# Optimization experiments

Measured on AMD Instinct MI355X. Metric: run time of the kernel, lower is better.

## Reference

```python
import jax, jax.numpy as jnp
import numpy as np
from jax import lax

CHUNK = 256  # points of the query set processed per step; intermediate is [B, CHUNK, M]


def _nn_min(x, y):
    """For each point in x [B,N,3], squared distance + index of nearest point in y [B,M,3].
    Chunked over N so the full [B,N,M] distance matrix is never materialized."""
    B, N, _ = x.shape
    y2 = jnp.sum(y * y, axis=-1)  # [B, M]
    K = N // CHUNK
    xr = jnp.swapaxes(x.reshape(B, K, CHUNK, 3), 0, 1)  # [K, B, CHUNK, 3]

    def chunk_fn(xc):  # xc: [B, CHUNK, 3]
        d = (jnp.sum(xc * xc, axis=-1)[..., None]
             - 2.0 * jnp.einsum('bcd,bmd->bcm', xc, y)
             + y2[:, None, :])  # [B, CHUNK, M]
        return jnp.min(d, axis=-1), jnp.argmin(d, axis=-1).astype(jnp.int32)

    dmin, idx = lax.map(chunk_fn, xr)  # [K, B, CHUNK]
    dmin = jnp.swapaxes(dmin, 0, 1).reshape(B, N)
    idx = jnp.swapaxes(idx, 0, 1).reshape(B, N)
    return dmin, idx


def setup_inputs() -> dict:
    key = jax.random.key(0)
    k1, k2 = jax.random.split(key)
    xyz1 = jax.random.normal(k1, (8, 16384, 3), dtype=jnp.float32)
    xyz2 = jax.random.normal(k2, (8, 16384, 3), dtype=jnp.float32)
    return {"xyz1": xyz1, "xyz2": xyz2}


def reference(xyz1, xyz2):
    dist1, idx1 = _nn_min(xyz1, xyz2)  # [B, N], [B, N]
    dist2, idx2 = _nn_min(xyz2, xyz1)  # [B, M], [B, M]
    return dist1, dist2, idx1, idx2
```

## Files before the change

### kernel.cpp

```cpp
#include <hip/hip_runtime.h>
#include <stdint.h>

#define BATCH 8
#define NPTS  16384
#define BN    (BATCH * NPTS)
#define CH    256
#define NCH   (NPTS / CH)
#define QPB   256
#define MARGIN 4.0e-3f

typedef float f32x16 __attribute__((ext_vector_type(16)));
typedef short s16x8  __attribute__((ext_vector_type(8)));

__device__ __forceinline__ uint16_t bfr(float x) {
    uint32_t u = __float_as_uint(x);
    return (uint16_t)((u + 0x7FFFu + ((u >> 16) & 1u)) >> 16);
}
__device__ __forceinline__ float bff(uint16_t s) {
    return __uint_as_float(((uint32_t)s) << 16);
}
__device__ __forceinline__ void split2(float v, uint16_t* a, uint16_t* b) {
    *a = bfr(v); *b = bfr(v - bff(*a));
}
__device__ __forceinline__ uint32_t pk2(uint16_t lo, uint16_t hi) {
    return (uint32_t)lo | ((uint32_t)hi << 16);
}
__device__ __forceinline__ uint32_t key32(float d) {
    uint32_t b = __float_as_uint(d);
    return (b & 0x80000000u) ? ~b : (b | 0x80000000u);
}
__device__ __forceinline__ float dec32(uint32_t k) {
    return __uint_as_float((k & 0x80000000u) ? (k ^ 0x80000000u) : ~k);
}

#define F16(M_) M_(0) M_(1) M_(2) M_(3) M_(4) M_(5) M_(6) M_(7) \
                M_(8) M_(9) M_(10) M_(11) M_(12) M_(13) M_(14) M_(15)

#define MIN3(a, b, c) fminf(fminf((a), (b)), (c))

__device__ __forceinline__ float fold16(const f32x16 a) {
    const float u0 = MIN3(a[0],  a[1],  a[2]);
    const float u1 = MIN3(a[3],  a[4],  a[5]);
    const float u2 = MIN3(a[6],  a[7],  a[8]);
    const float u3 = MIN3(a[9],  a[10], a[11]);
    const float u4 = MIN3(a[12], a[13], a[14]);
    const float v0 = MIN3(u0, u1, a[15]);
    const float v1 = MIN3(u2, u3, u4);
    return fminf(v0, v1);
}

__global__ __launch_bounds__(256) void enc_kernel(
    const float* __restrict__ Y, uint4* __restrict__ enc)
{
#pragma clang fp contract(off)
    const int g = blockIdx.x * 256 + threadIdx.x;
    const int b = g >> 14, p = g & (NPTS - 1);
    const float y0 = Y[(size_t)g * 3 + 0];
    const float y1 = Y[(size_t)g * 3 + 1];
    const float y2 = Y[(size_t)g * 3 + 2];
    const float ys = (y0 * y0 + y1 * y1) + y2 * y2;
    uint16_t Ya, Yb; split2(ys, &Ya, &Yb);
    uint16_t H0, M0; split2(-2.0f * y0, &H0, &M0);
    uint16_t H1, M1; split2(-2.0f * y1, &H1, &M1);
    uint16_t H2, M2; split2(-2.0f * y2, &H2, &M2);
    const uint16_t ONE = 0x3F80;
    const int ch = p >> 8, pp = p & (CH - 1);
    const size_t base = (size_t)(b * NCH + ch) * (2 * CH) + pp;
    enc[base]      = make_uint4(pk2(ONE, ONE), pk2(Ya, Yb), pk2(H0, M0), pk2(H0, M0));
    enc[base + CH] = make_uint4(pk2(H1, M1), pk2(H1, M1), pk2(H2, M2), pk2(H2, M2));
}

#define DECODE_DBX() \
    int dir, batch, kh, xblk; \
    { const int g = blockIdx.x; \
      const int s = 2 * (g & 7) + ((g >> 3) & 1); \
      dir = s >> 3; batch = s & 7; \
      if (ksplit == 2) { kh = (g >> 4) & 1; xblk = g >> 5; } \
      else             { kh = 0;            xblk = g >> 4; } }

#define STAGE(c, buf) { \
        const uint4* src_ = ep + (size_t)(c) * (2 * CH); \
        _Pragma("unroll") \
        for (int i_ = 0; i_ < 2; ++i_) \
            __builtin_amdgcn_global_load_lds( \
                (const __attribute__((address_space(1))) void*)(src_ + i_ * 256 + tid), \
                (__attribute__((address_space(3))) void*)&lds[buf][i_ * 256 + tid], \
                16, 0, 0); \
    }

#define MKQFR(dst, qq, qx0v, qx1v, qx2v, qxsv) { \
        const float* xp = Xp + (size_t)(bofs + (qq)) * 3; \
        qx0v = xp[0]; qx1v = xp[1]; qx2v = xp[2]; \
        qxsv = (qx0v * qx0v + qx1v * qx1v) + qx2v * qx2v; \
        uint16_t Xa, Xb; split2(qxsv, &Xa, &Xb); \
        uint16_t h0, m0; split2(qx0v, &h0, &m0); \
        uint16_t h1, m1; split2(qx1v, &h1, &m1); \
        uint16_t h2, m2; split2(qx2v, &h2, &m2); \
        const uint16_t ONE = 0x3F80; \
        if (hi == 0) { \
            dst[0]=(short)Xa; dst[1]=(short)Xb; dst[2]=(short)ONE; dst[3]=(short)ONE; \
            dst[4]=(short)h0; dst[5]=(short)h0; dst[6]=(short)m0;  dst[7]=(short)m0; \
        } else { \
            dst[0]=(short)h1; dst[1]=(short)h1; dst[2]=(short)m1;  dst[3]=(short)m1; \
            dst[4]=(short)h2; dst[5]=(short)h2; dst[6]=(short)m2;  dst[7]=(short)m2; \
        } }

__global__ __launch_bounds__(256, 4) void nn_sweep1(
    const float* __restrict__ xyz1, const float* __restrict__ xyz2,
    const uint4* __restrict__ encA, const uint4* __restrict__ encB,
    uint32_t* __restrict__ mkey, int ksplit)
{
#pragma clang fp contract(off)
    __shared__ uint4 lds[2][2 * CH];

    const int tid = threadIdx.x;
    const int l   = tid & 63;
    const int wv  = tid >> 6;
    const int col = l & 31;
    const int hi  = l >> 5;
    DECODE_DBX()

    const float* Xp = dir ? xyz2 : xyz1;
    const uint4* ep = (dir ? encB : encA) + (size_t)batch * (NCH * 2 * CH);
    const int bofs  = batch * NPTS;
    const int qbase = xblk * QPB + wv * 64;
    const int chalf = NCH / ksplit;
    const int c0 = kh * chalf, c1 = c0 + chalf;

    const f32x16 zf = {0.f,0.f,0.f,0.f,0.f,0.f,0.f,0.f,
                       0.f,0.f,0.f,0.f,0.f,0.f,0.f,0.f};

    s16x8 qfr0, qfr1;
    float qa0, qa1, qa2, qas, qb0, qb1, qb2, qbs;
    MKQFR(qfr0, qbase + col,      qa0, qa1, qa2, qas)
    MKQFR(qfr1, qbase + 32 + col, qb0, qb1, qb2, qbs)
    (void)qa0; (void)qb0;

    const int ldsb = hi * CH + col;

    float run0 = __builtin_inff(), run1 = __builtin_inff();
    STAGE(c0, 0);
    __syncthreads();
    int cur = 0;
    for (int c = c0; c < c1; ++c) {
        if (c + 1 < c1) STAGE(c + 1, cur ^ 1);
#pragma unroll
        for (int tp = 0; tp < CH / 32; ++tp) {
            const s16x8 pA = *(const s16x8*)&lds[cur][ldsb + tp * 32];
            const f32x16 a0 = __builtin_amdgcn_mfma_f32_32x32x16_bf16(pA, qfr0, zf, 0, 0, 0);
            run0 = fminf(run0, fold16(a0));
            const f32x16 a1 = __builtin_amdgcn_mfma_f32_32x32x16_bf16(pA, qfr1, zf, 0, 0, 0);
            run1 = fminf(run1, fold16(a1));
        }
        __syncthreads();
        cur ^= 1;
    }
    run0 = fminf(run0, __shfl_xor(run0, 32, 64));
    run1 = fminf(run1, __shfl_xor(run1, 32, 64));
    if (l < 32) {
        uint32_t* mp = mkey + (size_t)dir * BN + bofs + qbase;
        atomicMin(&mp[col],      key32(run0));
        atomicMin(&mp[32 + col], key32(run1));
    }
}

__global__ __launch_bounds__(256, 4) void nn_sweep2(
    const float* __restrict__ xyz1, const float* __restrict__ xyz2,
    const uint4* __restrict__ encA, const uint4* __restrict__ encB,
    const uint32_t* __restrict__ mkey, unsigned long long* __restrict__ gkeys,
    float* __restrict__ out, int ksplit)
{
#pragma clang fp contract(off)
    __shared__ uint4 lds[2][2 * CH];
    __shared__ unsigned long long keys[QPB];

    const int tid = threadIdx.x;
    const int l   = tid & 63;
    const int wv  = tid >> 6;
    const int col = l & 31;
    const int hi  = l >> 5;
    DECODE_DBX()

    const float* Xp = dir ? xyz2 : xyz1;
    const float* Yp = dir ? xyz1 : xyz2;
    const uint4* ep = (dir ? encB : encA) + (size_t)batch * (NCH * 2 * CH);
    const int bofs  = batch * NPTS;
    const int qbase = xblk * QPB + wv * 64;
    const int chalf = NCH / ksplit;
    const int c0 = kh * chalf, c1 = c0 + chalf;

    keys[tid] = ~0ull;

    const f32x16 zf = {0.f,0.f,0.f,0.f,0.f,0.f,0.f,0.f,
                       0.f,0.f,0.f,0.f,0.f,0.f,0.f,0.f};

    int rowpack[4] = {0, 0, 0, 0};
    {
        s16x8 pa = {0,0,0,0,0,0,0,0}, pb = {0,0,0,0,0,0,0,0};
        if (hi == 0) { pa[0] = (short)bfr((float)col); pb[0] = (short)0x3F80; }
        const f32x16 rowp = __builtin_amdgcn_mfma_f32_32x32x16_bf16(pa, pb, zf, 0, 0, 0);
#define PR(i) rowpack[(i) >> 2] |= ((int)rowp[i] & 0xFF) << (((i) & 3) * 8);
        F16(PR)
#undef PR
    }

    s16x8 qfr0, qfr1;
    float qa0, qa1, qa2, qas, qb0, qb1, qb2, qbs;
    MKQFR(qfr0, qbase + col,      qa0, qa1, qa2, qas)
    MKQFR(qfr1, qbase + 32 + col, qb0, qb1, qb2, qbs)

    float thr0, thr1;
    {
        const uint32_t* mp = mkey + (size_t)dir * BN + bofs + qbase;
        thr0 = dec32(mp[col]) + MARGIN;
        thr1 = dec32(mp[32 + col]) + MARGIN;
    }

    const int ldsb = hi * CH + col;

#define HITR(accv, jb, foff, thr, qx0, qx1, qx2, qxs, r) \
        if ((accv)[r] <= (thr)) { \
            const int jc = (jb) + ((rowpack[(r) >> 2] >> (((r) & 3) * 8)) & 0xFF); \
            const float* yq = Yp + (size_t)(bofs + jc) * 3; \
            const float py0 = yq[0], py1 = yq[1], py2 = yq[2]; \
            const float pys = (py0 * py0 + py1 * py1) + py2 * py2; \
            const float dd = ((qxs) - 2.0f * (((qx0) * py0 + (qx1) * py1) + (qx2) * py2)) + pys; \
            atomicMin(&keys[wv * 64 + (foff) + col], \
                      ((unsigned long long)key32(dd) << 32) | (uint32_t)jc); }
#define HIT(accv, jb, foff, thr, qx0, qx1, qx2, qxs) \
        if (fold16(accv) <= (thr)) { \
            HITR(accv, jb, foff, thr, qx0, qx1, qx2, qxs, 0) \
            HITR(accv, jb, foff, thr, qx0, qx1, qx2, qxs, 1) \
            HITR(accv, jb, foff, thr, qx0, qx1, qx2, qxs, 2) \
            HITR(accv, jb, foff, thr, qx0, qx1, qx2, qxs, 3) \
            HITR(accv, jb, foff, thr, qx0, qx1, qx2, qxs, 4) \
            HITR(accv, jb, foff, thr, qx0, qx1, qx2, qxs, 5) \
            HITR(accv, jb, foff, thr, qx0, qx1, qx2, qxs, 6) \
            HITR(accv, jb, foff, thr, qx0, qx1, qx2, qxs, 7) \
            HITR(accv, jb, foff, thr, qx0, qx1, qx2, qxs, 8) \
            HITR(accv, jb, foff, thr, qx0, qx1, qx2, qxs, 9) \
            HITR(accv, jb, foff, thr, qx0, qx1, qx2, qxs, 10) \
            HITR(accv, jb, foff, thr, qx0, qx1, qx2, qxs, 11) \
            HITR(accv, jb, foff, thr, qx0, qx1, qx2, qxs, 12) \
            HITR(accv, jb, foff, thr, qx0, qx1, qx2, qxs, 13) \
            HITR(accv, jb, foff, thr, qx0, qx1, qx2, qxs, 14) \
            HITR(accv, jb, foff, thr, qx0, qx1, qx2, qxs, 15) \
        }

    STAGE(c0, 0);
    __syncthreads();
    int cur = 0;
    for (int c = c0; c < c1; ++c) {
        if (c + 1 < c1) STAGE(c + 1, cur ^ 1);
#pragma unroll
        for (int tp = 0; tp < CH / 32; ++tp) {
            const s16x8 pA = *(const s16x8*)&lds[cur][ldsb + tp * 32];
            const int jb = c * CH + tp * 32;
            const f32x16 a0 = __builtin_amdgcn_mfma_f32_32x32x16_bf16(pA, qfr0, zf, 0, 0, 0);
            HIT(a0, jb, 0, thr0, qa0, qa1, qa2, qas)
            const f32x16 a1 = __builtin_amdgcn_mfma_f32_32x32x16_bf16(pA, qfr1, zf, 0, 0, 0);
            HIT(a1, jb, 32, thr1, qb0, qb1, qb2, qbs)
        }
        __syncthreads();
        cur ^= 1;
    }
#undef HIT
#undef HITR

    __syncthreads();
    {
        const unsigned long long m = keys[tid];
        const size_t gq = (size_t)dir * BN + bofs + (size_t)xblk * QPB + tid;
        if (ksplit == 2) {
            atomicMin(&gkeys[gq], m);
        } else {
            const uint32_t k32 = (uint32_t)(m >> 32);
            const size_t q = (size_t)bofs + (size_t)xblk * QPB + tid;
            out[(size_t)dir * BN + q]       = dec32(k32);
            out[(size_t)(2 + dir) * BN + q] = (float)(uint32_t)(m & 0xFFFFFFFFu);
        }
    }
}

__global__ __launch_bounds__(256) void writeout_k(
    const unsigned long long* __restrict__ gkeys, float* __restrict__ out)
{
    const size_t i = (size_t)blockIdx.x * 256 + threadIdx.x;
    const unsigned long long m = gkeys[i];
    const int dir = (int)(i / BN);
    const size_t q = i - (size_t)dir * BN;
    out[(size_t)dir * BN + q]       = dec32((uint32_t)(m >> 32));
    out[(size_t)(2 + dir) * BN + q] = (float)(uint32_t)(m & 0xFFFFFFFFu);
}

extern "C" void kernel_launch(void* const* d_in, const int* in_sizes, int n_in,
                              void* d_out, int out_size, void* d_ws, size_t ws_size,
                              hipStream_t stream) {
    const float* xyz1 = (const float*)d_in[0];
    const float* xyz2 = (const float*)d_in[1];
    float* out = (float*)d_out;

    uint4*    encA  = (uint4*)d_ws;
    uint4*    encB  = encA + (size_t)BN * 2;
    uint32_t* mkey  = (uint32_t*)(encB + (size_t)BN * 2);
    unsigned long long* gkeys = (unsigned long long*)(mkey + (size_t)2 * BN);

    enc_kernel<<<BN / 256, 256, 0, stream>>>(xyz2, encA);
    enc_kernel<<<BN / 256, 256, 0, stream>>>(xyz1, encB);

    if (ws_size >= (size_t)11 * 1024 * 1024) {
        hipMemsetAsync(mkey, 0xFF, (size_t)3 * 1024 * 1024, stream);
        nn_sweep1<<<2048, 256, 0, stream>>>(xyz1, xyz2, encA, encB, mkey, 2);
        nn_sweep2<<<2048, 256, 0, stream>>>(xyz1, xyz2, encA, encB, mkey, gkeys, out, 2);
        writeout_k<<<(2 * BN) / 256, 256, 0, stream>>>(gkeys, out);
    } else {
        hipMemsetAsync(mkey, 0xFF, (size_t)1024 * 1024, stream);
        nn_sweep1<<<1024, 256, 0, stream>>>(xyz1, xyz2, encA, encB, mkey, 1);
        nn_sweep2<<<1024, 256, 0, stream>>>(xyz1, xyz2, encA, encB, mkey, nullptr, out, 1);
    }
}
```

Measured before the change: 373.7 us.

## Switch distance encoding to three-way bf16 split with two MFMAs per tile

Replaces the two-term bf16 split of coordinates and norms with a three-term split, so each distance tile takes two chained MFMAs (K=32) instead of one and the staged encoding grows from 2 to 3 uint4 per point. The higher precision allows a much smaller refinement margin (8e-4 instead of 4e-3), meant to cut the number of candidates that fall through to the exact fp32 recheck and atomic updates in sweep2. The cost is twice the MFMA work, 50% more LDS and global traffic for the encoding, and a larger workspace requirement. The fallback path is restructured to run one direction at a time with a shared encoding buffer.

```diff
diff --git a/kernel.cpp b/kernel.cpp
--- a/kernel.cpp
+++ b/kernel.cpp
@@ -7,7 +7,7 @@
 #define CH    256
 #define NCH   (NPTS / CH)
 #define QPB   256
-#define MARGIN 4.0e-3f
+#define MARGIN 8.0e-4f
 
 typedef float f32x16 __attribute__((ext_vector_type(16)));
 typedef short s16x8  __attribute__((ext_vector_type(8)));
@@ -19,8 +19,10 @@
 __device__ __forceinline__ float bff(uint16_t s) {
     return __uint_as_float(((uint32_t)s) << 16);
 }
-__device__ __forceinline__ void split2(float v, uint16_t* a, uint16_t* b) {
-    *a = bfr(v); *b = bfr(v - bff(*a));
+__device__ __forceinline__ void split3(float v, uint16_t* a, uint16_t* b, uint16_t* c) {
+    *a = bfr(v);            const float f0 = bff(*a);
+    *b = bfr(v - f0);       const float f1 = bff(*b);
+    *c = bfr((v - f0) - f1);
 }
 __device__ __forceinline__ uint32_t pk2(uint16_t lo, uint16_t hi) {
     return (uint32_t)lo | ((uint32_t)hi << 16);
@@ -59,59 +61,63 @@
     const float y1 = Y[(size_t)g * 3 + 1];
     const float y2 = Y[(size_t)g * 3 + 2];
     const float ys = (y0 * y0 + y1 * y1) + y2 * y2;
-    uint16_t Ya, Yb; split2(ys, &Ya, &Yb);
-    uint16_t H0, M0; split2(-2.0f * y0, &H0, &M0);
-    uint16_t H1, M1; split2(-2.0f * y1, &H1, &M1);
-    uint16_t H2, M2; split2(-2.0f * y2, &H2, &M2);
+    uint16_t Sa, Sb, Sc;    split3(ys, &Sa, &Sb, &Sc);
+    uint16_t A0, B0, C0;    split3(-2.0f * y0, &A0, &B0, &C0);
+    uint16_t A1, B1, C1;    split3(-2.0f * y1, &A1, &B1, &C1);
+    uint16_t A2, B2, C2;    split3(-2.0f * y2, &A2, &B2, &C2);
     const uint16_t ONE = 0x3F80;
     const int ch = p >> 8, pp = p & (CH - 1);
-    const size_t base = (size_t)(b * NCH + ch) * (2 * CH) + pp;
-    enc[base]      = make_uint4(pk2(ONE, ONE), pk2(Ya, Yb), pk2(H0, M0), pk2(H0, M0));
-    enc[base + CH] = make_uint4(pk2(H1, M1), pk2(H1, M1), pk2(H2, M2), pk2(H2, M2));
+    const size_t base = (size_t)(b * NCH + ch) * (3 * CH) + pp;
+    enc[base]          = make_uint4(pk2(ONE, ONE), pk2(ONE, Sa), pk2(Sb, Sc), pk2(A0, A0));
+    enc[base + CH]     = make_uint4(pk2(A0, B0), pk2(B0, C0), pk2(A1, A1), pk2(A1, B1));
+    enc[base + 2 * CH] = make_uint4(pk2(B1, C1), pk2(A2, A2), pk2(A2, B2), pk2(B2, C2));
 }
 
 #define DECODE_DBX() \
     int dir, batch, kh, xblk; \
     { const int g = blockIdx.x; \
-      const int s = 2 * (g & 7) + ((g >> 3) & 1); \
-      dir = s >> 3; batch = s & 7; \
-      if (ksplit == 2) { kh = (g >> 4) & 1; xblk = g >> 5; } \
-      else             { kh = 0;            xblk = g >> 4; } }
+      if (ndir == 2) { const int s = 2 * (g & 7) + ((g >> 3) & 1); \
+          dir = s >> 3; batch = s & 7; kh = (g >> 4) & 1; xblk = g >> 5; } \
+      else { dir = dir0; batch = g & 7; kh = (g >> 3) & 1; xblk = g >> 4; } }
 
 #define STAGE(c, buf) { \
-        const uint4* src_ = ep + (size_t)(c) * (2 * CH); \
+        const uint4* src_ = ep + (size_t)(c) * (3 * CH); \
         _Pragma("unroll") \
-        for (int i_ = 0; i_ < 2; ++i_) \
+        for (int i_ = 0; i_ < 3; ++i_) \
             __builtin_amdgcn_global_load_lds( \
                 (const __attribute__((address_space(1))) void*)(src_ + i_ * 256 + tid), \
                 (__attribute__((address_space(3))) void*)&lds[buf][i_ * 256 + tid], \
                 16, 0, 0); \
     }
 
-#define MKQFR(dst, qq, qx0v, qx1v, qx2v, qxsv) { \
+#define MKQFR(qlo, qhi2, qq, qx0v, qx1v, qx2v, qxsv) { \
         const float* xp = Xp + (size_t)(bofs + (qq)) * 3; \
         qx0v = xp[0]; qx1v = xp[1]; qx2v = xp[2]; \
         qxsv = (qx0v * qx0v + qx1v * qx1v) + qx2v * qx2v; \
-        uint16_t Xa, Xb; split2(qxsv, &Xa, &Xb); \
-        uint16_t h0, m0; split2(qx0v, &h0, &m0); \
-        uint16_t h1, m1; split2(qx1v, &h1, &m1); \
-        uint16_t h2, m2; split2(qx2v, &h2, &m2); \
+        uint16_t Xa, Xb, Xc; split3(qxsv, &Xa, &Xb, &Xc); \
+        uint16_t h0, m0, l0; split3(qx0v, &h0, &m0, &l0); \
+        uint16_t h1, m1, l1; split3(qx1v, &h1, &m1, &l1); \
+        uint16_t h2, m2, l2; split3(qx2v, &h2, &m2, &l2); \
         const uint16_t ONE = 0x3F80; \
         if (hi == 0) { \
-            dst[0]=(short)Xa; dst[1]=(short)Xb; dst[2]=(short)ONE; dst[3]=(short)ONE; \
-            dst[4]=(short)h0; dst[5]=(short)h0; dst[6]=(short)m0;  dst[7]=(short)m0; \
+            qlo[0]=(short)Xa; qlo[1]=(short)Xb; qlo[2]=(short)Xc; qlo[3]=(short)ONE; \
+            qlo[4]=(short)ONE; qlo[5]=(short)ONE; qlo[6]=(short)h0; qlo[7]=(short)m0; \
+            qhi2[0]=(short)m1; qhi2[1]=(short)h1; qhi2[2]=(short)h2; qhi2[3]=(short)m2; \
+            qhi2[4]=(short)l2; qhi2[5]=(short)h2; qhi2[6]=(short)m2; qhi2[7]=(short)h2; \
         } else { \
-            dst[0]=(short)h1; dst[1]=(short)h1; dst[2]=(short)m1;  dst[3]=(short)m1; \
-            dst[4]=(short)h2; dst[5]=(short)h2; dst[6]=(short)m2;  dst[7]=(short)m2; \
+            qlo[0]=(short)l0; qlo[1]=(short)h0; qlo[2]=(short)m0; qlo[3]=(short)h0; \
+            qlo[4]=(short)h1; qlo[5]=(short)m1; qlo[6]=(short)l1; qlo[7]=(short)h1; \
+            qhi2[0]=0; qhi2[1]=0; qhi2[2]=0; qhi2[3]=0; \
+            qhi2[4]=0; qhi2[5]=0; qhi2[6]=0; qhi2[7]=0; \
         } }
 
 __global__ __launch_bounds__(256, 4) void nn_sweep1(
     const float* __restrict__ xyz1, const float* __restrict__ xyz2,
     const uint4* __restrict__ encA, const uint4* __restrict__ encB,
-    uint32_t* __restrict__ mkey, int ksplit)
+    uint32_t* __restrict__ mkey, int ndir, int dir0)
 {
 #pragma clang fp contract(off)
-    __shared__ uint4 lds[2][2 * CH];
+    __shared__ uint4 lds[2][3 * CH];
 
     const int tid = threadIdx.x;
     const int l   = tid & 63;
@@ -121,20 +127,20 @@
     DECODE_DBX()
 
     const float* Xp = dir ? xyz2 : xyz1;
-    const uint4* ep = (dir ? encB : encA) + (size_t)batch * (NCH * 2 * CH);
+    const uint4* ep = (dir ? encB : encA) + (size_t)batch * (NCH * 3 * CH);
     const int bofs  = batch * NPTS;
     const int qbase = xblk * QPB + wv * 64;
-    const int chalf = NCH / ksplit;
+    const int chalf = NCH / 2;
     const int c0 = kh * chalf, c1 = c0 + chalf;
 
     const f32x16 zf = {0.f,0.f,0.f,0.f,0.f,0.f,0.f,0.f,
                        0.f,0.f,0.f,0.f,0.f,0.f,0.f,0.f};
 
-    s16x8 qfr0, qfr1;
+    s16x8 q0lo, q0hi, q1lo, q1hi;
     float qa0, qa1, qa2, qas, qb0, qb1, qb2, qbs;
-    MKQFR(qfr0, qbase + col,      qa0, qa1, qa2, qas)
-    MKQFR(qfr1, qbase + 32 + col, qb0, qb1, qb2, qbs)
-    (void)qa0; (void)qb0;
+    MKQFR(q0lo, q0hi, qbase + col,      qa0, qa1, qa2, qas)
+    MKQFR(q1lo, q1hi, qbase + 32 + col, qb0, qb1, qb2, qbs)
+    (void)qa0; (void)qb0; (void)qas; (void)qbs;
 
     const int ldsb = hi * CH + col;
 
@@ -147,9 +153,12 @@
 #pragma unroll
         for (int tp = 0; tp < CH / 32; ++tp) {
             const s16x8 pA = *(const s16x8*)&lds[cur][ldsb + tp * 32];
-            const f32x16 a0 = __builtin_amdgcn_mfma_f32_32x32x16_bf16(pA, qfr0, zf, 0, 0, 0);
+            const s16x8 pC = *(const s16x8*)&lds[cur][2 * CH + tp * 32 + col];
+            f32x16 a0 = __builtin_amdgcn_mfma_f32_32x32x16_bf16(pA, q0lo, zf, 0, 0, 0);
+            f32x16 a1 = __builtin_amdgcn_mfma_f32_32x32x16_bf16(pA, q1lo, zf, 0, 0, 0);
+            a0 = __builtin_amdgcn_mfma_f32_32x32x16_bf16(pC, q0hi, a0, 0, 0, 0);
+            a1 = __builtin_amdgcn_mfma_f32_32x32x16_bf16(pC, q1hi, a1, 0, 0, 0);
             run0 = fminf(run0, fold16(a0));
-            const f32x16 a1 = __builtin_amdgcn_mfma_f32_32x32x16_bf16(pA, qfr1, zf, 0, 0, 0);
             run1 = fminf(run1, fold16(a1));
         }
         __syncthreads();
@@ -168,10 +177,10 @@
     const float* __restrict__ xyz1, const float* __restrict__ xyz2,
     const uint4* __restrict__ encA, const uint4* __restrict__ encB,
     const uint32_t* __restrict__ mkey, unsigned long long* __restrict__ gkeys,
-    float* __restrict__ out, int ksplit)
+    int ndir, int dir0)
 {
 #pragma clang fp contract(off)
-    __shared__ uint4 lds[2][2 * CH];
+    __shared__ uint4 lds[2][3 * CH];
     __shared__ unsigned long long keys[QPB];
 
     const int tid = threadIdx.x;
@@ -183,10 +192,10 @@
 
     const float* Xp = dir ? xyz2 : xyz1;
     const float* Yp = dir ? xyz1 : xyz2;
-    const uint4* ep = (dir ? encB : encA) + (size_t)batch * (NCH * 2 * CH);
+    const uint4* ep = (dir ? encB : encA) + (size_t)batch * (NCH * 3 * CH);
     const int bofs  = batch * NPTS;
     const int qbase = xblk * QPB + wv * 64;
-    const int chalf = NCH / ksplit;
+    const int chalf = NCH / 2;
     const int c0 = kh * chalf, c1 = c0 + chalf;
 
     keys[tid] = ~0ull;
@@ -204,10 +213,10 @@
 #undef PR
     }
 
-    s16x8 qfr0, qfr1;
+    s16x8 q0lo, q0hi, q1lo, q1hi;
     float qa0, qa1, qa2, qas, qb0, qb1, qb2, qbs;
-    MKQFR(qfr0, qbase + col,      qa0, qa1, qa2, qas)
-    MKQFR(qfr1, qbase + 32 + col, qb0, qb1, qb2, qbs)
+    MKQFR(q0lo, q0hi, qbase + col,      qa0, qa1, qa2, qas)
+    MKQFR(q1lo, q1hi, qbase + 32 + col, qb0, qb1, qb2, qbs)
 
     float thr0, thr1;
     {
@@ -255,10 +264,13 @@
 #pragma unroll
         for (int tp = 0; tp < CH / 32; ++tp) {
             const s16x8 pA = *(const s16x8*)&lds[cur][ldsb + tp * 32];
+            const s16x8 pC = *(const s16x8*)&lds[cur][2 * CH + tp * 32 + col];
             const int jb = c * CH + tp * 32;
-            const f32x16 a0 = __builtin_amdgcn_mfma_f32_32x32x16_bf16(pA, qfr0, zf, 0, 0, 0);
-            HIT(a0, jb, 0, thr0, qa0, qa1, qa2, qas)
-            const f32x16 a1 = __builtin_amdgcn_mfma_f32_32x32x16_bf16(pA, qfr1, zf, 0, 0, 0);
+            f32x16 a0 = __builtin_amdgcn_mfma_f32_32x32x16_bf16(pA, q0lo, zf, 0, 0, 0);
+            f32x16 a1 = __builtin_amdgcn_mfma_f32_32x32x16_bf16(pA, q1lo, zf, 0, 0, 0);
+            a0 = __builtin_amdgcn_mfma_f32_32x32x16_bf16(pC, q0hi, a0, 0, 0, 0);
+            a1 = __builtin_amdgcn_mfma_f32_32x32x16_bf16(pC, q1hi, a1, 0, 0, 0);
+            HIT(a0, jb, 0,  thr0, qa0, qa1, qa2, qas)
             HIT(a1, jb, 32, thr1, qb0, qb1, qb2, qbs)
         }
         __syncthreads();
@@ -271,14 +283,7 @@
     {
         const unsigned long long m = keys[tid];
         const size_t gq = (size_t)dir * BN + bofs + (size_t)xblk * QPB + tid;
-        if (ksplit == 2) {
-            atomicMin(&gkeys[gq], m);
-        } else {
-            const uint32_t k32 = (uint32_t)(m >> 32);
-            const size_t q = (size_t)bofs + (size_t)xblk * QPB + tid;
-            out[(size_t)dir * BN + q]       = dec32(k32);
-            out[(size_t)(2 + dir) * BN + q] = (float)(uint32_t)(m & 0xFFFFFFFFu);
-        }
+        atomicMin(&gkeys[gq], m);
     }
 }
 
@@ -300,22 +305,30 @@
     const float* xyz2 = (const float*)d_in[1];
     float* out = (float*)d_out;
 
-    uint4*    encA  = (uint4*)d_ws;
-    uint4*    encB  = encA + (size_t)BN * 2;
-    uint32_t* mkey  = (uint32_t*)(encB + (size_t)BN * 2);
-    unsigned long long* gkeys = (unsigned long long*)(mkey + (size_t)2 * BN);
-
-    enc_kernel<<<BN / 256, 256, 0, stream>>>(xyz2, encA);
-    enc_kernel<<<BN / 256, 256, 0, stream>>>(xyz1, encB);
-
-    if (ws_size >= (size_t)11 * 1024 * 1024) {
+    if (ws_size >= (size_t)16 * 1024 * 1024) {
+        uint4*    encA = (uint4*)d_ws;
+        uint4*    encB = encA + (size_t)3 * BN;
+        uint32_t* mkey = (uint32_t*)(encB + (size_t)3 * BN);
+        unsigned long long* gkeys = (unsigned long long*)(mkey + (size_t)2 * BN);
+
+        enc_kernel<<<BN / 256, 256, 0, stream>>>(xyz2, encA);
+        enc_kernel<<<BN / 256, 256, 0, stream>>>(xyz1, encB);
         hipMemsetAsync(mkey, 0xFF, (size_t)3 * 1024 * 1024, stream);
-        nn_sweep1<<<2048, 256, 0, stream>>>(xyz1, xyz2, encA, encB, mkey, 2);
-        nn_sweep2<<<2048, 256, 0, stream>>>(xyz1, xyz2, encA, encB, mkey, gkeys, out, 2);
+        nn_sweep1<<<2048, 256, 0, stream>>>(xyz1, xyz2, encA, encB, mkey, 2, 0);
+        nn_sweep2<<<2048, 256, 0, stream>>>(xyz1, xyz2, encA, encB, mkey, gkeys, 2, 0);
         writeout_k<<<(2 * BN) / 256, 256, 0, stream>>>(gkeys, out);
     } else {
-        hipMemsetAsync(mkey, 0xFF, (size_t)1024 * 1024, stream);
-        nn_sweep1<<<1024, 256, 0, stream>>>(xyz1, xyz2, encA, encB, mkey, 1);
-        nn_sweep2<<<1024, 256, 0, stream>>>(xyz1, xyz2, encA, encB, mkey, nullptr, out, 1);
-    }
-}
+        uint4*    enc  = (uint4*)d_ws;
+        uint32_t* mkey = (uint32_t*)(enc + (size_t)3 * BN);
+        unsigned long long* gkeys = (unsigned long long*)(mkey + (size_t)2 * BN);
+
+        hipMemsetAsync(mkey, 0xFF, (size_t)3 * 1024 * 1024, stream);
+        enc_kernel<<<BN / 256, 256, 0, stream>>>(xyz2, enc);
+        nn_sweep1<<<1024, 256, 0, stream>>>(xyz1, xyz2, enc, enc, mkey, 1, 0);
+        nn_sweep2<<<1024, 256, 0, stream>>>(xyz1, xyz2, enc, enc, mkey, gkeys, 1, 0);
+        enc_kernel<<<BN / 256, 256, 0, stream>>>(xyz1, enc);
+        nn_sweep1<<<1024, 256, 0, stream>>>(xyz1, xyz2, enc, enc, mkey, 1, 1);
+        nn_sweep2<<<1024, 256, 0, stream>>>(xyz1, xyz2, enc, enc, mkey, gkeys, 1, 1);
+        writeout_k<<<(2 * BN) / 256, 256, 0, stream>>>(gkeys, out);
+    }
+}
```

After: 491.5 us. 1.32x slower.

## Fuse two-pass NN sweep into single pass with running threshold

Applied to the files above, without the earlier changes.

Replaces the two-pass scheme (a first sweep computing per-query minima, then a second sweep re-running the MFMAs to refine candidates) with one fused kernel. It seeds a running minimum from the first chunk and refines candidates on the fly against a running threshold plus a margin. Candidate refinement now reads precomputed float4 (x,y,z,|y|^2) instead of recomputing from xyz. This halves MFMA work, but early in the sweep the threshold is looser, so more candidates may take the exact-refinement path with LDS atomics.

```diff
diff --git a/kernel.cpp b/kernel.cpp
--- a/kernel.cpp
+++ b/kernel.cpp
@@ -50,7 +50,8 @@
 }
 
 __global__ __launch_bounds__(256) void enc_kernel(
-    const float* __restrict__ Y, uint4* __restrict__ enc)
+    const float* __restrict__ Y, uint4* __restrict__ enc,
+    float4* __restrict__ y4)
 {
 #pragma clang fp contract(off)
     const int g = blockIdx.x * 256 + threadIdx.x;
@@ -68,15 +69,15 @@
     const size_t base = (size_t)(b * NCH + ch) * (2 * CH) + pp;
     enc[base]      = make_uint4(pk2(ONE, ONE), pk2(Ya, Yb), pk2(H0, M0), pk2(H0, M0));
     enc[base + CH] = make_uint4(pk2(H1, M1), pk2(H1, M1), pk2(H2, M2), pk2(H2, M2));
+    y4[g] = make_float4(y0, y1, y2, ys);
 }
 
 #define DECODE_DBX() \
     int dir, batch, kh, xblk; \
     { const int g = blockIdx.x; \
-      const int s = 2 * (g & 7) + ((g >> 3) & 1); \
-      dir = s >> 3; batch = s & 7; \
-      if (ksplit == 2) { kh = (g >> 4) & 1; xblk = g >> 5; } \
-      else             { kh = 0;            xblk = g >> 4; } }
+      if (ndir == 2) { const int s = 2 * (g & 7) + ((g >> 3) & 1); \
+          dir = s >> 3; batch = s & 7; kh = (g >> 4) & 1; xblk = g >> 5; } \
+      else { dir = dir0; batch = g & 7; kh = (g >> 3) & 1; xblk = g >> 4; } }
 
 #define STAGE(c, buf) { \
         const uint4* src_ = ep + (size_t)(c) * (2 * CH); \
@@ -105,13 +106,15 @@
             dst[4]=(short)h2; dst[5]=(short)h2; dst[6]=(short)m2;  dst[7]=(short)m2; \
         } }
 
-__global__ __launch_bounds__(256, 4) void nn_sweep1(
+__global__ __launch_bounds__(256, 4) void nn_fused(
     const float* __restrict__ xyz1, const float* __restrict__ xyz2,
     const uint4* __restrict__ encA, const uint4* __restrict__ encB,
-    uint32_t* __restrict__ mkey, int ksplit)
+    const float4* __restrict__ y4A, const float4* __restrict__ y4B,
+    unsigned long long* __restrict__ gkeys, int ndir, int dir0)
 {
 #pragma clang fp contract(off)
     __shared__ uint4 lds[2][2 * CH];
+    __shared__ unsigned long long keys[QPB];
 
     const int tid = threadIdx.x;
     const int l   = tid & 63;
@@ -120,73 +123,12 @@
     const int hi  = l >> 5;
     DECODE_DBX()
 
-    const float* Xp = dir ? xyz2 : xyz1;
-    const uint4* ep = (dir ? encB : encA) + (size_t)batch * (NCH * 2 * CH);
+    const float*  Xp = dir ? xyz2 : xyz1;
+    const uint4*  ep = (dir ? encB : encA) + (size_t)batch * (NCH * 2 * CH);
+    const float4* Y4 = (dir ? y4B : y4A) + (size_t)batch * NPTS;
     const int bofs  = batch * NPTS;
     const int qbase = xblk * QPB + wv * 64;
-    const int chalf = NCH / ksplit;
-    const int c0 = kh * chalf, c1 = c0 + chalf;
-
-    const f32x16 zf = {0.f,0.f,0.f,0.f,0.f,0.f,0.f,0.f,
-                       0.f,0.f,0.f,0.f,0.f,0.f,0.f,0.f};
-
-    s16x8 qfr0, qfr1;
-    float qa0, qa1, qa2, qas, qb0, qb1, qb2, qbs;
-    MKQFR(qfr0, qbase + col,      qa0, qa1, qa2, qas)
-    MKQFR(qfr1, qbase + 32 + col, qb0, qb1, qb2, qbs)
-    (void)qa0; (void)qb0;
-
-    const int ldsb = hi * CH + col;
-
-    float run0 = __builtin_inff(), run1 = __builtin_inff();
-    STAGE(c0, 0);
-    __syncthreads();
-    int cur = 0;
-    for (int c = c0; c < c1; ++c) {
-        if (c + 1 < c1) STAGE(c + 1, cur ^ 1);
-#pragma unroll
-        for (int tp = 0; tp < CH / 32; ++tp) {
-            const s16x8 pA = *(const s16x8*)&lds[cur][ldsb + tp * 32];
-            const f32x16 a0 = __builtin_amdgcn_mfma_f32_32x32x16_bf16(pA, qfr0, zf, 0, 0, 0);
-            run0 = fminf(run0, fold16(a0));
-            const f32x16 a1 = __builtin_amdgcn_mfma_f32_32x32x16_bf16(pA, qfr1, zf, 0, 0, 0);
-            run1 = fminf(run1, fold16(a1));
-        }
-        __syncthreads();
-        cur ^= 1;
-    }
-    run0 = fminf(run0, __shfl_xor(run0, 32, 64));
-    run1 = fminf(run1, __shfl_xor(run1, 32, 64));
-    if (l < 32) {
-        uint32_t* mp = mkey + (size_t)dir * BN + bofs + qbase;
-        atomicMin(&mp[col],      key32(run0));
-        atomicMin(&mp[32 + col], key32(run1));
-    }
-}
-
-__global__ __launch_bounds__(256, 4) void nn_sweep2(
-    const float* __restrict__ xyz1, const float* __restrict__ xyz2,
-    const uint4* __restrict__ encA, const uint4* __restrict__ encB,
-    const uint32_t* __restrict__ mkey, unsigned long long* __restrict__ gkeys,
-    float* __restrict__ out, int ksplit)
-{
-#pragma clang fp contract(off)
-    __shared__ uint4 lds[2][2 * CH];
-    __shared__ unsigned long long keys[QPB];
-
-    const int tid = threadIdx.x;
-    const int l   = tid & 63;
-    const int wv  = tid >> 6;
-    const int col = l & 31;
-    const int hi  = l >> 5;
-    DECODE_DBX()
-
-    const float* Xp = dir ? xyz2 : xyz1;
-    const float* Yp = dir ? xyz1 : xyz2;
-    const uint4* ep = (dir ? encB : encA) + (size_t)batch * (NCH * 2 * CH);
-    const int bofs  = batch * NPTS;
-    const int qbase = xblk * QPB + wv * 64;
-    const int chalf = NCH / ksplit;
+    const int chalf = NCH / 2;
     const int c0 = kh * chalf, c1 = c0 + chalf;
 
     keys[tid] = ~0ull;
@@ -209,26 +151,32 @@
     MKQFR(qfr0, qbase + col,      qa0, qa1, qa2, qas)
     MKQFR(qfr1, qbase + 32 + col, qb0, qb1, qb2, qbs)
 
-    float thr0, thr1;
-    {
-        const uint32_t* mp = mkey + (size_t)dir * BN + bofs + qbase;
-        thr0 = dec32(mp[col]) + MARGIN;
-        thr1 = dec32(mp[32 + col]) + MARGIN;
-    }
-
     const int ldsb = hi * CH + col;
+
+    float run0 = __builtin_inff(), run1 = __builtin_inff();
+
+    STAGE(c0, 0);
+    __syncthreads();
+#pragma unroll
+    for (int tp = 0; tp < CH / 32; ++tp) {
+        const s16x8 pA = *(const s16x8*)&lds[0][ldsb + tp * 32];
+        const f32x16 a0 = __builtin_amdgcn_mfma_f32_32x32x16_bf16(pA, qfr0, zf, 0, 0, 0);
+        run0 = fminf(run0, fold16(a0));
+        const f32x16 a1 = __builtin_amdgcn_mfma_f32_32x32x16_bf16(pA, qfr1, zf, 0, 0, 0);
+        run1 = fminf(run1, fold16(a1));
+    }
+    run0 = fminf(run0, __shfl_xor(run0, 32, 64));
+    run1 = fminf(run1, __shfl_xor(run1, 32, 64));
 
 #define HITR(accv, jb, foff, thr, qx0, qx1, qx2, qxs, r) \
         if ((accv)[r] <= (thr)) { \
             const int jc = (jb) + ((rowpack[(r) >> 2] >> (((r) & 3) * 8)) & 0xFF); \
-            const float* yq = Yp + (size_t)(bofs + jc) * 3; \
-            const float py0 = yq[0], py1 = yq[1], py2 = yq[2]; \
-            const float pys = (py0 * py0 + py1 * py1) + py2 * py2; \
-            const float dd = ((qxs) - 2.0f * (((qx0) * py0 + (qx1) * py1) + (qx2) * py2)) + pys; \
+            const float4 yv = Y4[jc]; \
+            const float dd = ((qxs) - 2.0f * (((qx0) * yv.x + (qx1) * yv.y) + (qx2) * yv.z)) + yv.w; \
             atomicMin(&keys[wv * 64 + (foff) + col], \
                       ((unsigned long long)key32(dd) << 32) | (uint32_t)jc); }
 #define HIT(accv, jb, foff, thr, qx0, qx1, qx2, qxs) \
-        if (fold16(accv) <= (thr)) { \
+        { \
             HITR(accv, jb, foff, thr, qx0, qx1, qx2, qxs, 0) \
             HITR(accv, jb, foff, thr, qx0, qx1, qx2, qxs, 1) \
             HITR(accv, jb, foff, thr, qx0, qx1, qx2, qxs, 2) \
@@ -247,8 +195,6 @@
             HITR(accv, jb, foff, thr, qx0, qx1, qx2, qxs, 15) \
         }
 
-    STAGE(c0, 0);
-    __syncthreads();
     int cur = 0;
     for (int c = c0; c < c1; ++c) {
         if (c + 1 < c1) STAGE(c + 1, cur ^ 1);
@@ -256,11 +202,23 @@
         for (int tp = 0; tp < CH / 32; ++tp) {
             const s16x8 pA = *(const s16x8*)&lds[cur][ldsb + tp * 32];
             const int jb = c * CH + tp * 32;
-            const f32x16 a0 = __builtin_amdgcn_mfma_f32_32x32x16_bf16(pA, qfr0, zf, 0, 0, 0);
-            HIT(a0, jb, 0, thr0, qa0, qa1, qa2, qas)
-            const f32x16 a1 = __builtin_amdgcn_mfma_f32_32x32x16_bf16(pA, qfr1, zf, 0, 0, 0);
-            HIT(a1, jb, 32, thr1, qb0, qb1, qb2, qbs)
+            {
+                const f32x16 a0 = __builtin_amdgcn_mfma_f32_32x32x16_bf16(pA, qfr0, zf, 0, 0, 0);
+                const float f0 = fold16(a0);
+                run0 = fminf(run0, f0);
+                const float t0v = run0 + MARGIN;
+                if (f0 <= t0v) HIT(a0, jb, 0, t0v, qa0, qa1, qa2, qas)
+            }
+            {
+                const f32x16 a1 = __builtin_amdgcn_mfma_f32_32x32x16_bf16(pA, qfr1, zf, 0, 0, 0);
+                const float f1 = fold16(a1);
+                run1 = fminf(run1, f1);
+                const float t1v = run1 + MARGIN;
+                if (f1 <= t1v) HIT(a1, jb, 32, t1v, qb0, qb1, qb2, qbs)
+            }
         }
+        run0 = fminf(run0, __shfl_xor(run0, 32, 64));
+        run1 = fminf(run1, __shfl_xor(run1, 32, 64));
         __syncthreads();
         cur ^= 1;
     }
@@ -271,14 +229,7 @@
     {
         const unsigned long long m = keys[tid];
         const size_t gq = (size_t)dir * BN + bofs + (size_t)xblk * QPB + tid;
-        if (ksplit == 2) {
-            atomicMin(&gkeys[gq], m);
-        } else {
-            const uint32_t k32 = (uint32_t)(m >> 32);
-            const size_t q = (size_t)bofs + (size_t)xblk * QPB + tid;
-            out[(size_t)dir * BN + q]       = dec32(k32);
-            out[(size_t)(2 + dir) * BN + q] = (float)(uint32_t)(m & 0xFFFFFFFFu);
-        }
+        atomicMin(&gkeys[gq], m);
     }
 }
 
@@ -300,22 +251,31 @@
     const float* xyz2 = (const float*)d_in[1];
     float* out = (float*)d_out;
 
-    uint4*    encA  = (uint4*)d_ws;
-    uint4*    encB  = encA + (size_t)BN * 2;
-    uint32_t* mkey  = (uint32_t*)(encB + (size_t)BN * 2);
-    unsigned long long* gkeys = (unsigned long long*)(mkey + (size_t)2 * BN);
-
-    enc_kernel<<<BN / 256, 256, 0, stream>>>(xyz2, encA);
-    enc_kernel<<<BN / 256, 256, 0, stream>>>(xyz1, encB);
-
-    if (ws_size >= (size_t)11 * 1024 * 1024) {
-        hipMemsetAsync(mkey, 0xFF, (size_t)3 * 1024 * 1024, stream);
-        nn_sweep1<<<2048, 256, 0, stream>>>(xyz1, xyz2, encA, encB, mkey, 2);
-        nn_sweep2<<<2048, 256, 0, stream>>>(xyz1, xyz2, encA, encB, mkey, gkeys, out, 2);
+    if (ws_size >= (size_t)15 * 1024 * 1024) {
+        uint4*  encA = (uint4*)d_ws;
+        uint4*  encB = encA + (size_t)2 * BN;
+        float4* y4A  = (float4*)(encB + (size_t)2 * BN);
+        float4* y4B  = y4A + BN;
+        unsigned long long* gkeys = (unsigned long long*)(y4B + BN);
+
+        enc_kernel<<<BN / 256, 256, 0, stream>>>(xyz2, encA, y4A);
+        enc_kernel<<<BN / 256, 256, 0, stream>>>(xyz1, encB, y4B);
+        hipMemsetAsync(gkeys, 0xFF, (size_t)2 * 1024 * 1024, stream);
+        nn_fused<<<2048, 256, 0, stream>>>(xyz1, xyz2, encA, encB, y4A, y4B,
+                                           gkeys, 2, 0);
         writeout_k<<<(2 * BN) / 256, 256, 0, stream>>>(gkeys, out);
     } else {
-        hipMemsetAsync(mkey, 0xFF, (size_t)1024 * 1024, stream);
-        nn_sweep1<<<1024, 256, 0, stream>>>(xyz1, xyz2, encA, encB, mkey, 1);
-        nn_sweep2<<<1024, 256, 0, stream>>>(xyz1, xyz2, encA, encB, mkey, nullptr, out, 1);
-    }
-}
+        uint4*  enc = (uint4*)d_ws;
+        float4* y4  = (float4*)(enc + (size_t)2 * BN);
+        unsigned long long* gkeys = (unsigned long long*)(y4 + BN);
+
+        hipMemsetAsync(gkeys, 0xFF, (size_t)2 * 1024 * 1024, stream);
+        enc_kernel<<<BN / 256, 256, 0, stream>>>(xyz2, enc, y4);
+        nn_fused<<<1024, 256, 0, stream>>>(xyz1, xyz2, enc, enc, y4, y4,
+                                           gkeys, 1, 0);
+        enc_kernel<<<BN / 256, 256, 0, stream>>>(xyz1, enc, y4);
+        nn_fused<<<1024, 256, 0, stream>>>(xyz1, xyz2, enc, enc, y4, y4,
+                                           gkeys, 1, 1);
+        writeout_k<<<(2 * BN) / 256, 256, 0, stream>>>(gkeys, out);
+    }
+}
```

Measured after the change: 413.8 us. +10.7%, slower.
